# Performance work log

Hardware: AMD Instinct MI355X
Metric: run time of the kernel (lower is better)

The kernel has to match this reference:

```python
import jax, jax.numpy as jnp
import numpy as np


def setup_inputs() -> dict:
    key = jax.random.key(0)
    k1, k2 = jax.random.split(key)
    B, G = 32, 512
    center = jax.random.normal(k1, (B, G, 6), dtype=jnp.float32)
    lrf = jax.random.normal(k2, (B, G, 3, 3), dtype=jnp.float32)
    return {"center": center, "lrf": lrf}


def reference(center, lrf):
    # center: [B, G, 6], lrf: [B, G, 3, 3]
    center_pos = center[:, :, 0:3]                       # [B, G, 3]
    # diff[b, i, j, c] = center_pos[b, j, c] - center_pos[b, i, c]
    diff = center_pos[:, None, :, :] - center_pos[:, :, None, :]  # [B, G, G, 3]
    # rel_pos[b, i, j, k] = sum_c diff[b, i, j, c] * lrf[b, i, c, k]
    rel_pos = jnp.einsum('bijc,bick->bijk', diff, lrf)   # [B, G, G, 3]
    # rel_ori[b, i, j] = lrf[b, i]^T @ lrf[b, j]
    rel_ori = jnp.einsum('bikm,bjkn->bijmn', lrf, lrf)   # [B, G, G, 3, 3]
    return (rel_pos, rel_ori)
```

## Files before the change

### kernel.cpp

```cpp
#include <hip/hip_runtime.h>


#define G_ 512
#define NB 32

typedef float f4v __attribute__((ext_vector_type(4)));

__global__ __launch_bounds__(256, 8) void relposori_kernel(
    const float* __restrict__ center,
    const float* __restrict__ lrf,
    float* __restrict__ out_pos,
    float* __restrict__ out_ori)
{
    __shared__ float s[3072];
    float* s_pos = s;
    float* s_ori = s + 768;

    int tid = threadIdx.x;
    int p   = blockIdx.x;
    int bi0 = p << 3;
    int b   = bi0 >> 9;

    const float* cb = center + (size_t)b * (G_ * 6);
    const float* lb = lrf    + (size_t)b * (G_ * 9);

    for (int rr = 0; rr < 8; ++rr) {
        int bi = bi0 + rr;

        const float* ci = center + (size_t)bi * 6;
        const float* li = lrf    + (size_t)bi * 9;
        float ci0 = ci[0], ci1 = ci[1], ci2 = ci[2];
        float li_[9];
#pragma unroll
        for (int t = 0; t < 9; ++t) li_[t] = li[t];

#pragma unroll
        for (int half = 0; half < 2; ++half) {
            int j = (half << 8) | tid;
            const float* cj = cb + j * 6;
            const float* lj = lb + j * 9;
            float d0 = cj[0] - ci0, d1 = cj[1] - ci1, d2 = cj[2] - ci2;
            float lj_[9];
#pragma unroll
            for (int t = 0; t < 9; ++t) lj_[t] = lj[t];

#pragma unroll
            for (int k = 0; k < 3; ++k)
                s_pos[tid * 3 + k] = d0 * li_[k] + d1 * li_[3 + k] + d2 * li_[6 + k];

#pragma unroll
            for (int m = 0; m < 3; ++m)
#pragma unroll
                for (int n = 0; n < 3; ++n)
                    s_ori[tid * 9 + m * 3 + n] = li_[m]     * lj_[n]
                                               + li_[3 + m] * lj_[3 + n]
                                               + li_[6 + m] * lj_[6 + n];

            asm volatile("s_waitcnt lgkmcnt(0)" ::: "memory");
            __builtin_amdgcn_s_barrier();

            const f4v* s4 = (const f4v*)s;
            f4v* op4 = (f4v*)out_pos + ((size_t)bi * 384  + (size_t)half * 192);
            f4v* oo4 = (f4v*)out_ori + ((size_t)bi * 1152 + (size_t)half * 576);
#pragma unroll
            for (int it = 0; it < 3; ++it) {
                int t = tid + (it << 8);
                if (t < 192) op4[t]       = s4[t];
                else         oo4[t - 192] = s4[t];
            }

            asm volatile("s_waitcnt lgkmcnt(0)" ::: "memory");
            __builtin_amdgcn_s_barrier();
        }
    }
}

extern "C" void kernel_launch(void* const* d_in, const int* in_sizes, int n_in,
                              void* d_out, int out_size, void* d_ws, size_t ws_size,
                              hipStream_t stream) {
    const float* center = (const float*)d_in[0];
    const float* lrf    = (const float*)d_in[1];
    float* out = (float*)d_out;

    const int B = 32;
    const size_t n_pos = (size_t)B * G_ * G_ * 3;
    float* out_pos = out;
    float* out_ori = out + n_pos;

    dim3 grid(2048);
    dim3 block(256);
    hipLaunchKernelGGL(relposori_kernel, grid, block, 0, stream,
                       center, lrf, out_pos, out_ori);
}
```

Before: 83.76 us.

## Launch one row per block and prefetch second half loads before stores

```diff
diff --git a/kernel.cpp b/kernel.cpp
--- a/kernel.cpp
+++ b/kernel.cpp
@@ -2,9 +2,9 @@
 
 
 #define G_ 512
-#define NB 32
 
 typedef float f4v __attribute__((ext_vector_type(4)));
+typedef float f4u __attribute__((ext_vector_type(4), aligned(4)));
 
 __global__ __launch_bounds__(256, 8) void relposori_kernel(
     const float* __restrict__ center,
@@ -16,61 +16,94 @@
     float* s_pos = s;
     float* s_ori = s + 768;
 
+    int bi  = blockIdx.x;
+    int b   = bi >> 9;
     int tid = threadIdx.x;
-    int p   = blockIdx.x;
-    int bi0 = p << 3;
-    int b   = bi0 >> 9;
 
     const float* cb = center + (size_t)b * (G_ * 6);
     const float* lb = lrf    + (size_t)b * (G_ * 9);
 
-    for (int rr = 0; rr < 8; ++rr) {
-        int bi = bi0 + rr;
+    const float* ci = center + (size_t)bi * 6;
+    const float* li = lrf    + (size_t)bi * 9;
+    float ci0 = ci[0], ci1 = ci[1], ci2 = ci[2];
+    float li_[9];
+#pragma unroll
+    for (int t = 0; t < 9; ++t) li_[t] = li[t];
 
-        const float* ci = center + (size_t)bi * 6;
-        const float* li = lrf    + (size_t)bi * 9;
-        float ci0 = ci[0], ci1 = ci[1], ci2 = ci[2];
-        float li_[9];
+    const float* cj0 = cb + tid * 6;
+    const float* lj0 = lb + tid * 9;
+    f4u c03 = *(const f4u*)cj0;
+    f4u l03 = *(const f4u*)lj0;
+    f4u l47 = *(const f4u*)(lj0 + 4);
+    float l8 = lj0[8];
+
+    {
+        float d0 = c03.x - ci0, d1 = c03.y - ci1, d2 = c03.z - ci2;
+        float lj_[9] = { l03.x, l03.y, l03.z, l03.w,
+                         l47.x, l47.y, l47.z, l47.w, l8 };
 #pragma unroll
-        for (int t = 0; t < 9; ++t) li_[t] = li[t];
+        for (int k = 0; k < 3; ++k)
+            s_pos[tid * 3 + k] = d0 * li_[k] + d1 * li_[3 + k] + d2 * li_[6 + k];
+#pragma unroll
+        for (int m = 0; m < 3; ++m)
+#pragma unroll
+            for (int n = 0; n < 3; ++n)
+                s_ori[tid * 9 + m * 3 + n] = li_[m]     * lj_[n]
+                                           + li_[3 + m] * lj_[3 + n]
+                                           + li_[6 + m] * lj_[6 + n];
+    }
+    __syncthreads();
 
+    const float* cj1 = cb + (256 + tid) * 6;
+    const float* lj1 = lb + (256 + tid) * 9;
+    f4u c03b = *(const f4u*)cj1;
+    f4u l03b = *(const f4u*)lj1;
+    f4u l47b = *(const f4u*)(lj1 + 4);
+    float l8b = lj1[8];
+    asm volatile("" ::: "memory");
+
+    {
+        const f4v* s4 = (const f4v*)s;
+        f4v* op4 = (f4v*)out_pos + (size_t)bi * 384;
+        f4v* oo4 = (f4v*)out_ori + (size_t)bi * 1152;
 #pragma unroll
-        for (int half = 0; half < 2; ++half) {
-            int j = (half << 8) | tid;
-            const float* cj = cb + j * 6;
-            const float* lj = lb + j * 9;
-            float d0 = cj[0] - ci0, d1 = cj[1] - ci1, d2 = cj[2] - ci2;
-            float lj_[9];
+        for (int it = 0; it < 3; ++it) {
+            int t = tid + (it << 8);
+            if (t < 192) op4[t]       = s4[t];
+            else         oo4[t - 192] = s4[t];
+        }
+    }
+
+    asm volatile("" ::: "memory");
+    __builtin_amdgcn_s_barrier();
+
+    {
+        float d0 = c03b.x - ci0, d1 = c03b.y - ci1, d2 = c03b.z - ci2;
+        float lj_[9] = { l03b.x, l03b.y, l03b.z, l03b.w,
+                         l47b.x, l47b.y, l47b.z, l47b.w, l8b };
 #pragma unroll
-            for (int t = 0; t < 9; ++t) lj_[t] = lj[t];
+        for (int k = 0; k < 3; ++k)
+            s_pos[tid * 3 + k] = d0 * li_[k] + d1 * li_[3 + k] + d2 * li_[6 + k];
+#pragma unroll
+        for (int m = 0; m < 3; ++m)
+#pragma unroll
+            for (int n = 0; n < 3; ++n)
+                s_ori[tid * 9 + m * 3 + n] = li_[m]     * lj_[n]
+                                           + li_[3 + m] * lj_[3 + n]
+                                           + li_[6 + m] * lj_[6 + n];
+    }
+    asm volatile("s_waitcnt lgkmcnt(0)" ::: "memory");
+    __builtin_amdgcn_s_barrier();
 
+    {
+        const f4v* s4 = (const f4v*)s;
+        f4v* op4 = (f4v*)out_pos + (size_t)bi * 384  + 192;
+        f4v* oo4 = (f4v*)out_ori + (size_t)bi * 1152 + 576;
 #pragma unroll
-            for (int k = 0; k < 3; ++k)
-                s_pos[tid * 3 + k] = d0 * li_[k] + d1 * li_[3 + k] + d2 * li_[6 + k];
-
-#pragma unroll
-            for (int m = 0; m < 3; ++m)
-#pragma unroll
-                for (int n = 0; n < 3; ++n)
-                    s_ori[tid * 9 + m * 3 + n] = li_[m]     * lj_[n]
-                                               + li_[3 + m] * lj_[3 + n]
-                                               + li_[6 + m] * lj_[6 + n];
-
-            asm volatile("s_waitcnt lgkmcnt(0)" ::: "memory");
-            __builtin_amdgcn_s_barrier();
-
-            const f4v* s4 = (const f4v*)s;
-            f4v* op4 = (f4v*)out_pos + ((size_t)bi * 384  + (size_t)half * 192);
-            f4v* oo4 = (f4v*)out_ori + ((size_t)bi * 1152 + (size_t)half * 576);
-#pragma unroll
-            for (int it = 0; it < 3; ++it) {
-                int t = tid + (it << 8);
-                if (t < 192) op4[t]       = s4[t];
-                else         oo4[t - 192] = s4[t];
-            }
-
-            asm volatile("s_waitcnt lgkmcnt(0)" ::: "memory");
-            __builtin_amdgcn_s_barrier();
+        for (int it = 0; it < 3; ++it) {
+            int t = tid + (it << 8);
+            if (t < 192) op4[t]       = s4[t];
+            else         oo4[t - 192] = s4[t];
         }
     }
 }
@@ -87,7 +120,7 @@
     float* out_pos = out;
     float* out_ori = out + n_pos;
 
-    dim3 grid(2048);
+    dim3 grid(B * G_);
     dim3 block(256);
     hipLaunchKernelGGL(relposori_kernel, grid, block, 0, stream,
                        center, lrf, out_pos, out_ori);
```

Measured after the change: 78.50 us. 6.3% less time.
